# Optimization experiments

Hardware: AMD Instinct MI355X
Metric: run time of the kernel (lower is better)

Reference implementation:

```python
import jax, jax.numpy as jnp
import numpy as np

B, Q, K, D = 32, 1024, 1024, 64
MASK_VAL = -1000000.0  # matches torch source's -1e6 fill


def setup_inputs() -> dict:
    key = jax.random.key(0)
    kq, kk, kv, kl = jax.random.split(key, 4)
    return {
        "queries": jax.random.normal(kq, (B, Q, D), dtype=jnp.float32),
        "keys": jax.random.normal(kk, (B, K, D), dtype=jnp.float32),
        "values": jax.random.normal(kv, (B, K, D), dtype=jnp.float32),
        "valid_lens": jax.random.randint(kl, (B,), 1, K + 1, dtype=jnp.int64),
    }


def reference(queries, keys, values, valid_lens):
    d = queries.shape[-1]
    # [B, Q, K] scores
    scores = jnp.einsum("bqd,bkd->bqk", queries, keys) / jnp.sqrt(jnp.asarray(d, queries.dtype))
    # 1D valid_lens -> same length mask for every query row of a batch element
    kv_pos = jnp.arange(scores.shape[-1])  # [K]
    mask = kv_pos[None, None, :] < valid_lens[:, None, None]  # [B, 1, K] broadcast
    scores = jnp.where(mask, scores, MASK_VAL)
    attn = jax.nn.softmax(scores, axis=-1)
    # dropout p=0.0 -> identity
    return jnp.einsum("bqk,bkd->bqd", attn, values)
```

## Files before the change

### kernel.cpp

```cpp
#include <hip/hip_runtime.h>
#include <hip/hip_bf16.h>

#define NB 32
#define NQ 1024
#define NK 1024
#define ND 64
#define BK 64
#define M_FIX 16.0f

typedef __attribute__((ext_vector_type(8))) __bf16 bf16x8;
typedef __attribute__((ext_vector_type(8))) short  s16x8;
typedef __attribute__((ext_vector_type(4))) short  s16x4;
typedef __attribute__((ext_vector_type(4))) float  f32x4;
typedef __attribute__((ext_vector_type(2))) int    i32x2;

static __device__ __forceinline__ short f2bf(float f) {
  unsigned u = __builtin_bit_cast(unsigned, f);
  u += 0x7fffu + ((u >> 16) & 1u);
  return (short)(u >> 16);
}

static __device__ __forceinline__ int swzoff(int row, int gcol) {
  return row * 64 + (((gcol ^ (row & 7)) & 7) << 3);
}

#define GLD_LDS16(gp, lp)                                              \
  __builtin_amdgcn_global_load_lds(                                    \
      (const __attribute__((address_space(1))) void*)(gp),             \
      (__attribute__((address_space(3))) void*)(lp), 16, 0, 0)

#define MFMA16(acc, va_, vb_)                                          \
  asm("v_mfma_f32_16x16x16_bf16 %0, %1, %2, %0"                        \
      : "+v"(acc) : "v"(va_), "v"(vb_))

__launch_bounds__(256)
__global__ void prep_kv(const float* __restrict__ Kp, const float* __restrict__ Vp,
                        const int* __restrict__ VLp,
                        short* __restrict__ Kb, short* __restrict__ Vt) {
  __shared__ __align__(16) short T[64 * 72];
  const int wg = blockIdx.x;
  const int b  = wg >> 4;
  const int kt = wg & 15;

  const bool is64 = (VLp[1] == 0);
  const int  len  = is64 ? VLp[2 * b] : VLp[b];
  if (kt * 64 >= len) return;

  const int tid = threadIdx.x;

  {
    const int key = tid >> 2, d0 = (tid & 3) * 16, g0 = (tid & 3) * 2;
    const float* src = Kp + ((size_t)(b * NK + kt * 64 + key)) * ND + d0;
    short out[16];
#pragma unroll
    for (int i = 0; i < 16; i += 4) {
      float4 v = *(const float4*)(src + i);
      out[i] = f2bf(v.x); out[i + 1] = f2bf(v.y);
      out[i + 2] = f2bf(v.z); out[i + 3] = f2bf(v.w);
    }
    short* dtile = Kb + ((size_t)(b * 16 + kt)) * 4096;
    *(s16x8*)&dtile[swzoff(key, g0)]     = *(const s16x8*)out;
    *(s16x8*)&dtile[swzoff(key, g0 + 1)] = *(const s16x8*)(out + 8);
  }

  {
    const int vkey = tid & 63, vd0 = (tid >> 6) * 16;
    const float* src = Vp + ((size_t)(b * NK + kt * 64 + vkey)) * ND + vd0;
#pragma unroll
    for (int i = 0; i < 4; ++i) {
      float4 v = *(const float4*)(src + i * 4);
      T[(vd0 + i * 4 + 0) * 72 + vkey] = f2bf(v.x);
      T[(vd0 + i * 4 + 1) * 72 + vkey] = f2bf(v.y);
      T[(vd0 + i * 4 + 2) * 72 + vkey] = f2bf(v.z);
      T[(vd0 + i * 4 + 3) * 72 + vkey] = f2bf(v.w);
    }
  }
  __syncthreads();
  {
    const int d = tid >> 2, q4 = tid & 3;
    short* vtile = Vt + ((size_t)(b * 16 + kt)) * 4096;
    const short* s = &T[d * 72 + q4 * 16];
#pragma unroll
    for (int i = 0; i < 4; ++i)
      *(s16x4*)&vtile[d * 64 + (((4 * q4 + i) ^ (d & 15)) << 2)] =
          *(const s16x4*)(s + 4 * i);
  }
}

__launch_bounds__(512, 4)
__global__ void attn_fwd(const float* __restrict__ Qp,
                         const short* __restrict__ Kb,
                         const short* __restrict__ Vt,
                         const int* __restrict__ VLp,
                         float* __restrict__ Op) {
  __shared__ __align__(16) short SM[32768];
  char* smb = (char*)SM;

  const int wg  = blockIdx.x;
  const int swz = (wg & 7) * 64 + (wg >> 3);
  const int b   = swz >> 4;
  const int qb  = swz & 15;

  const int tid  = threadIdx.x;
  const int wid  = tid >> 6;
  const int lane = tid & 63;
  const int l16  = lane & 15;
  const int grp  = lane >> 4;
  const int esw  = l16 & 7;
  const int qgrp = wid >> 1;
  const int par  = wid & 1;

  const bool is64 = (VLp[1] == 0);
  const int  len  = is64 ? VLp[2 * b] : VLp[b];
  const int  ntiles = (len + BK - 1) >> 6;
  const int  nsup   = (ntiles + 1) >> 1;
  const int  remLast = len - ((ntiles - 1) << 6);

  const float qscale = 0.125f * 1.44269504088896341f;

  bf16x8 qf[2];
  {
    const float* qsrc = Qp + ((size_t)(b * NQ + qb * 64 + qgrp * 16 + l16)) * ND + grp * 8;
#pragma unroll
    for (int k2 = 0; k2 < 2; ++k2) {
      float4 a = *(const float4*)(qsrc + k2 * 32);
      float4 c = *(const float4*)(qsrc + k2 * 32 + 4);
      s16x8 t;
      t[0] = f2bf(a.x * qscale); t[1] = f2bf(a.y * qscale);
      t[2] = f2bf(a.z * qscale); t[3] = f2bf(a.w * qscale);
      t[4] = f2bf(c.x * qscale); t[5] = f2bf(c.y * qscale);
      t[6] = f2bf(c.z * qscale); t[7] = f2bf(c.w * qscale);
      qf[k2] = __builtin_bit_cast(bf16x8, t);
    }
  }

  const int ka0 = par * 8192 + l16 * 128 + (((0 + grp) ^ esw) << 4);
  const int ka1 = par * 8192 + l16 * 128 + (((4 + grp) ^ esw) << 4);
  int van[4];
#pragma unroll
  for (int n = 0; n < 4; ++n)
    van[n] = 32768 + par * 8192 + l16 * 128 + (((4 * n + grp) ^ l16) << 3);

  const char* kgp = (const char*)(Kb + (size_t)b * 16 * 4096) + tid * 16;
  const char* vgp = (const char*)(Vt + (size_t)b * 16 * 4096) + tid * 16;
  const int dstW = wid * 1024;

  const f32x4 minit = {-M_FIX, -M_FIX, -M_FIX, -M_FIX};
  const f32x4 vzero = {0.f, 0.f, 0.f, 0.f};
  f32x4 oacc[4];
#pragma unroll
  for (int i = 0; i < 4; ++i) oacc[i] = vzero;
  float lrun = 0.f;

  int bufB = 0;

  GLD_LDS16(kgp,        smb + dstW);
  GLD_LDS16(kgp + 8192, smb + 8192 + dstW);
  GLD_LDS16(vgp,        smb + 32768 + dstW);
  GLD_LDS16(vgp + 8192, smb + 40960 + dstW);
  kgp += 16384; vgp += 16384;

  for (int it = 0; it < nsup; ++it) {
    asm volatile("s_waitcnt vmcnt(0)" ::: "memory");
    __builtin_amdgcn_sched_barrier(0);
    __builtin_amdgcn_s_barrier();
    __builtin_amdgcn_sched_barrier(0);

    if (it + 1 < nsup) {
      const int nb = bufB ^ 16384;
      GLD_LDS16(kgp,        smb + nb + dstW);
      GLD_LDS16(kgp + 8192, smb + nb + 8192 + dstW);
      GLD_LDS16(vgp,        smb + 32768 + nb + dstW);
      GLD_LDS16(vgp + 8192, smb + 32768 + nb + 8192 + dstW);
      kgp += 16384; vgp += 16384;
    }

    const int myt = 2 * it + par;
    if (myt < ntiles) {
      f32x4 sc[4];
      __builtin_amdgcn_s_setprio(1);
#pragma unroll
      for (int n = 0; n < 4; ++n) {
        bf16x8 kf0 = __builtin_bit_cast(bf16x8,
            *(const s16x8*)(smb + bufB + ka0 + n * 2048));
        bf16x8 kf1 = __builtin_bit_cast(bf16x8,
            *(const s16x8*)(smb + bufB + ka1 + n * 2048));
        f32x4 acc = __builtin_amdgcn_mfma_f32_16x16x32_bf16(kf0, qf[0], minit, 0, 0, 0);
        acc = __builtin_amdgcn_mfma_f32_16x16x32_bf16(kf1, qf[1], acc, 0, 0, 0);
        sc[n] = acc;
      }
      __builtin_amdgcn_s_setprio(0);

      i32x2 pk[4];
      if (myt == ntiles - 1) {
#pragma unroll
        for (int n = 0; n < 4; ++n) {
#pragma unroll
          for (int r = 0; r < 4; ++r) {
            float x = (n * 16 + grp * 4 + r < remLast) ? sc[n][r] : -128.0f;
            float pv = exp2f(x);
            sc[n][r] = pv;
            lrun += pv;
          }
          int plo, phi;
          asm("v_cvt_pk_bf16_f32 %0, %1, %2" : "=v"(plo) : "v"(sc[n][0]), "v"(sc[n][1]));
          asm("v_cvt_pk_bf16_f32 %0, %1, %2" : "=v"(phi) : "v"(sc[n][2]), "v"(sc[n][3]));
          pk[n][0] = plo; pk[n][1] = phi;
        }
      } else {
#pragma unroll
        for (int n = 0; n < 4; ++n) {
#pragma unroll
          for (int r = 0; r < 4; ++r) {
            float pv = exp2f(sc[n][r]);
            sc[n][r] = pv;
            lrun += pv;
          }
          int plo, phi;
          asm("v_cvt_pk_bf16_f32 %0, %1, %2" : "=v"(plo) : "v"(sc[n][0]), "v"(sc[n][1]));
          asm("v_cvt_pk_bf16_f32 %0, %1, %2" : "=v"(phi) : "v"(sc[n][2]), "v"(sc[n][3]));
          pk[n][0] = plo; pk[n][1] = phi;
        }
      }
      __builtin_amdgcn_sched_barrier(0);

      __builtin_amdgcn_s_setprio(1);
#pragma unroll
      for (int m = 0; m < 4; ++m) {
        i32x2 vf0 = *(const i32x2*)(smb + bufB + van[0] + m * 2048);
        i32x2 vf1 = *(const i32x2*)(smb + bufB + van[1] + m * 2048);
        i32x2 vf2 = *(const i32x2*)(smb + bufB + van[2] + m * 2048);
        i32x2 vf3 = *(const i32x2*)(smb + bufB + van[3] + m * 2048);
        MFMA16(oacc[m], vf0, pk[0]);
        MFMA16(oacc[m], vf1, pk[1]);
        MFMA16(oacc[m], vf2, pk[2]);
        MFMA16(oacc[m], vf3, pk[3]);
      }
      __builtin_amdgcn_s_setprio(0);
    }

    bufB ^= 16384;
  }

  __builtin_amdgcn_sched_barrier(0);
  asm volatile("s_nop 7\n\ts_nop 7" ::: "memory");

  __syncthreads();
  float* CB = (float*)SM;
  const int crow = qgrp * 64 + lane;
  if (par == 1) {
    float* dst = CB + (size_t)crow * 20;
#pragma unroll
    for (int m = 0; m < 4; ++m) *(f32x4*)(dst + m * 4) = oacc[m];
    dst[16] = lrun;
  }
  __syncthreads();
  if (par == 0) {
    const float* src = CB + (size_t)crow * 20;
#pragma unroll
    for (int m = 0; m < 4; ++m) oacc[m] += *(const f32x4*)(src + m * 4);
    float l = lrun + src[16];
    l += __shfl_xor(l, 16);
    l += __shfl_xor(l, 32);
    const float inv = 1.0f / l;

    float* obase = Op + ((size_t)(b * NQ + qb * 64 + qgrp * 16 + l16)) * ND;
#pragma unroll
    for (int m = 0; m < 4; ++m) {
      float4 o = {oacc[m][0] * inv, oacc[m][1] * inv,
                  oacc[m][2] * inv, oacc[m][3] * inv};
      *(float4*)(obase + m * 16 + grp * 4) = o;
    }
  }
}

extern "C" void kernel_launch(void* const* d_in, const int* in_sizes, int n_in,
                              void* d_out, int out_size, void* d_ws, size_t ws_size,
                              hipStream_t stream) {
  const float* Qp = (const float*)d_in[0];
  const float* Kp = (const float*)d_in[1];
  const float* Vp = (const float*)d_in[2];
  const int*   VL = (const int*)d_in[3];
  float* Op = (float*)d_out;

  short* Kb = (short*)d_ws;
  short* Vt = Kb + (size_t)NB * NK * ND;

  prep_kv<<<dim3(NB * 16), dim3(256), 0, stream>>>(Kp, Vp, VL, Kb, Vt);
  attn_fwd<<<dim3(NB * 16), dim3(512), 0, stream>>>(Qp, Kb, Vt, VL, Op);
}
```

Measured before the change: 29.57 us.

## Shrink key tiles to 32 and use triple-buffered LDS with prefetch depth two

Key tiles shrink from 64 to 32 keys, with K and V prepacked into 2048-element sub-tiles and a new V swizzle so each lane reads one 16-byte LDS vector per MFMA pair. The attention kernel moves from a double buffer to a three-slot ring and keeps two loads in flight using vmcnt(2), so global-to-LDS transfer overlaps more compute. LDS drops from 64 KB to 48 KB, which may allow more resident workgroups. The cost is twice as many loop iterations and barriers per key range, and finer masking granularity on the last tile.

```diff
diff --git a/kernel.cpp b/kernel.cpp
--- a/kernel.cpp
+++ b/kernel.cpp
@@ -5,23 +5,19 @@
 #define NQ 1024
 #define NK 1024
 #define ND 64
-#define BK 64
 #define M_FIX 16.0f
 
 typedef __attribute__((ext_vector_type(8))) __bf16 bf16x8;
 typedef __attribute__((ext_vector_type(8))) short  s16x8;
 typedef __attribute__((ext_vector_type(4))) short  s16x4;
 typedef __attribute__((ext_vector_type(4))) float  f32x4;
+typedef __attribute__((ext_vector_type(4))) int    i32x4;
 typedef __attribute__((ext_vector_type(2))) int    i32x2;
 
 static __device__ __forceinline__ short f2bf(float f) {
   unsigned u = __builtin_bit_cast(unsigned, f);
   u += 0x7fffu + ((u >> 16) & 1u);
   return (short)(u >> 16);
-}
-
-static __device__ __forceinline__ int swzoff(int row, int gcol) {
-  return row * 64 + (((gcol ^ (row & 7)) & 7) << 3);
 }
 
 #define GLD_LDS16(gp, lp)                                              \
@@ -50,6 +46,7 @@
 
   {
     const int key = tid >> 2, d0 = (tid & 3) * 16, g0 = (tid & 3) * 2;
+    const int row = key & 31, st = key >> 5;
     const float* src = Kp + ((size_t)(b * NK + kt * 64 + key)) * ND + d0;
     short out[16];
 #pragma unroll
@@ -58,9 +55,9 @@
       out[i] = f2bf(v.x); out[i + 1] = f2bf(v.y);
       out[i + 2] = f2bf(v.z); out[i + 3] = f2bf(v.w);
     }
-    short* dtile = Kb + ((size_t)(b * 16 + kt)) * 4096;
-    *(s16x8*)&dtile[swzoff(key, g0)]     = *(const s16x8*)out;
-    *(s16x8*)&dtile[swzoff(key, g0 + 1)] = *(const s16x8*)(out + 8);
+    short* dtile = Kb + ((size_t)(b * 32 + kt * 2 + st)) * 2048;
+    *(s16x8*)&dtile[row * 64 + (((g0    ) ^ (row & 7)) << 3)] = *(const s16x8*)out;
+    *(s16x8*)&dtile[row * 64 + (((g0 + 1) ^ (row & 7)) << 3)] = *(const s16x8*)(out + 8);
   }
 
   {
@@ -78,12 +75,13 @@
   __syncthreads();
   {
     const int d = tid >> 2, q4 = tid & 3;
-    short* vtile = Vt + ((size_t)(b * 16 + kt)) * 4096;
+    const int st = q4 >> 1, half = q4 & 1;
+    short* vtile = Vt + ((size_t)(b * 32 + kt * 2 + st)) * 2048;
     const short* s = &T[d * 72 + q4 * 16];
 #pragma unroll
-    for (int i = 0; i < 4; ++i)
-      *(s16x4*)&vtile[d * 64 + (((4 * q4 + i) ^ (d & 15)) << 2)] =
-          *(const s16x4*)(s + 4 * i);
+    for (int g = 0; g < 4; ++g)
+      *(s16x4*)&vtile[d * 32 + (((g ^ (d & 3)) & 3) << 3) + half * 4] =
+          *(const s16x4*)(s + 4 * g);
   }
 }
 
@@ -93,7 +91,7 @@
                          const short* __restrict__ Vt,
                          const int* __restrict__ VLp,
                          float* __restrict__ Op) {
-  __shared__ __align__(16) short SM[32768];
+  __shared__ __align__(16) short SM[24576];
   char* smb = (char*)SM;
 
   const int wg  = blockIdx.x;
@@ -107,14 +105,15 @@
   const int l16  = lane & 15;
   const int grp  = lane >> 4;
   const int esw  = l16 & 7;
+  const int e3   = l16 & 3;
   const int qgrp = wid >> 1;
   const int par  = wid & 1;
 
   const bool is64 = (VLp[1] == 0);
   const int  len  = is64 ? VLp[2 * b] : VLp[b];
-  const int  ntiles = (len + BK - 1) >> 6;
+  const int  ntiles = (len + 31) >> 5;
   const int  nsup   = (ntiles + 1) >> 1;
-  const int  remLast = len - ((ntiles - 1) << 6);
+  const int  remLast = len - ((ntiles - 1) << 5);
 
   const float qscale = 0.125f * 1.44269504088896341f;
 
@@ -134,15 +133,12 @@
     }
   }
 
-  const int ka0 = par * 8192 + l16 * 128 + (((0 + grp) ^ esw) << 4);
-  const int ka1 = par * 8192 + l16 * 128 + (((4 + grp) ^ esw) << 4);
-  int van[4];
-#pragma unroll
-  for (int n = 0; n < 4; ++n)
-    van[n] = 32768 + par * 8192 + l16 * 128 + (((4 * n + grp) ^ l16) << 3);
-
-  const char* kgp = (const char*)(Kb + (size_t)b * 16 * 4096) + tid * 16;
-  const char* vgp = (const char*)(Vt + (size_t)b * 16 * 4096) + tid * 16;
+  const int kOff0 = par * 4096 + l16 * 128 + (((0 + grp) ^ esw) << 4);
+  const int kOff1 = par * 4096 + l16 * 128 + (((4 + grp) ^ esw) << 4);
+  const int vOff  = par * 4096 + l16 * 64 + ((((grp ^ e3) & 3)) << 4);
+
+  const char* kgp = (const char*)(Kb + (size_t)b * 32 * 2048) + tid * 16;
+  const char* vgp = (const char*)(Vt + (size_t)b * 32 * 2048) + tid * 16;
   const int dstW = wid * 1024;
 
   const f32x4 minit = {-M_FIX, -M_FIX, -M_FIX, -M_FIX};
@@ -152,49 +148,54 @@
   for (int i = 0; i < 4; ++i) oacc[i] = vzero;
   float lrun = 0.f;
 
-  int bufB = 0;
-
-  GLD_LDS16(kgp,        smb + dstW);
-  GLD_LDS16(kgp + 8192, smb + 8192 + dstW);
-  GLD_LDS16(vgp,        smb + 32768 + dstW);
-  GLD_LDS16(vgp + 8192, smb + 40960 + dstW);
-  kgp += 16384; vgp += 16384;
+  GLD_LDS16(kgp, smb + dstW);
+  GLD_LDS16(vgp, smb + 24576 + dstW);
+  kgp += 8192; vgp += 8192;
+  if (nsup > 1) {
+    GLD_LDS16(kgp, smb + 8192 + dstW);
+    GLD_LDS16(vgp, smb + 32768 + dstW);
+    kgp += 8192; vgp += 8192;
+  }
+
+  int kbCur = 0;
+  int kbDst = 16384;
 
   for (int it = 0; it < nsup; ++it) {
-    asm volatile("s_waitcnt vmcnt(0)" ::: "memory");
+    if (it + 1 < nsup) {
+      asm volatile("s_waitcnt vmcnt(2)" ::: "memory");
+    } else {
+      asm volatile("s_waitcnt vmcnt(0)" ::: "memory");
+    }
     __builtin_amdgcn_sched_barrier(0);
     __builtin_amdgcn_s_barrier();
     __builtin_amdgcn_sched_barrier(0);
 
-    if (it + 1 < nsup) {
-      const int nb = bufB ^ 16384;
-      GLD_LDS16(kgp,        smb + nb + dstW);
-      GLD_LDS16(kgp + 8192, smb + nb + 8192 + dstW);
-      GLD_LDS16(vgp,        smb + 32768 + nb + dstW);
-      GLD_LDS16(vgp + 8192, smb + 32768 + nb + 8192 + dstW);
-      kgp += 16384; vgp += 16384;
+    if (it + 2 < nsup) {
+      GLD_LDS16(kgp, smb + kbDst + dstW);
+      GLD_LDS16(vgp, smb + 24576 + kbDst + dstW);
+      kgp += 8192; vgp += 8192;
     }
 
     const int myt = 2 * it + par;
     if (myt < ntiles) {
-      f32x4 sc[4];
+      f32x4 sc[2];
       __builtin_amdgcn_s_setprio(1);
 #pragma unroll
-      for (int n = 0; n < 4; ++n) {
+      for (int n = 0; n < 2; ++n) {
         bf16x8 kf0 = __builtin_bit_cast(bf16x8,
-            *(const s16x8*)(smb + bufB + ka0 + n * 2048));
+            *(const s16x8*)(smb + kbCur + kOff0 + n * 2048));
         bf16x8 kf1 = __builtin_bit_cast(bf16x8,
-            *(const s16x8*)(smb + bufB + ka1 + n * 2048));
+            *(const s16x8*)(smb + kbCur + kOff1 + n * 2048));
         f32x4 acc = __builtin_amdgcn_mfma_f32_16x16x32_bf16(kf0, qf[0], minit, 0, 0, 0);
         acc = __builtin_amdgcn_mfma_f32_16x16x32_bf16(kf1, qf[1], acc, 0, 0, 0);
         sc[n] = acc;
       }
       __builtin_amdgcn_s_setprio(0);
 
-      i32x2 pk[4];
+      i32x2 pk[2];
       if (myt == ntiles - 1) {
 #pragma unroll
-        for (int n = 0; n < 4; ++n) {
+        for (int n = 0; n < 2; ++n) {
 #pragma unroll
           for (int r = 0; r < 4; ++r) {
             float x = (n * 16 + grp * 4 + r < remLast) ? sc[n][r] : -128.0f;
@@ -209,7 +210,7 @@
         }
       } else {
 #pragma unroll
-        for (int n = 0; n < 4; ++n) {
+        for (int n = 0; n < 2; ++n) {
 #pragma unroll
           for (int r = 0; r < 4; ++r) {
             float pv = exp2f(sc[n][r]);
@@ -227,19 +228,17 @@
       __builtin_amdgcn_s_setprio(1);
 #pragma unroll
       for (int m = 0; m < 4; ++m) {
-        i32x2 vf0 = *(const i32x2*)(smb + bufB + van[0] + m * 2048);
-        i32x2 vf1 = *(const i32x2*)(smb + bufB + van[1] + m * 2048);
-        i32x2 vf2 = *(const i32x2*)(smb + bufB + van[2] + m * 2048);
-        i32x2 vf3 = *(const i32x2*)(smb + bufB + van[3] + m * 2048);
-        MFMA16(oacc[m], vf0, pk[0]);
-        MFMA16(oacc[m], vf1, pk[1]);
-        MFMA16(oacc[m], vf2, pk[2]);
-        MFMA16(oacc[m], vf3, pk[3]);
+        i32x4 w = *(const i32x4*)(smb + 24576 + kbCur + vOff + m * 1024);
+        i32x2 vlo = {w[0], w[1]};
+        i32x2 vhi = {w[2], w[3]};
+        MFMA16(oacc[m], vlo, pk[0]);
+        MFMA16(oacc[m], vhi, pk[1]);
       }
       __builtin_amdgcn_s_setprio(0);
     }
 
-    bufB ^= 16384;
+    kbCur = (kbCur == 16384) ? 0 : kbCur + 8192;
+    kbDst = (kbDst == 16384) ? 0 : kbDst + 8192;
   }
 
   __builtin_amdgcn_sched_barrier(0);
```

Measured after the change: 30.04 us. Within noise of the previous version (+1.6%).
